# Performance work log

Hardware: AMD Instinct MI355X
Metric: run time of the kernel (lower is better)

Reference implementation:

```python
import jax, jax.numpy as jnp
import numpy as np

DIM = 1024
PRUNE_RATE = 1.0


def setup_inputs() -> dict:
    key = jax.random.key(0)
    k1, k2 = jax.random.split(key)
    x = jax.random.normal(k1, (8, 4096, DIM), dtype=jnp.float32)
    mask_param = jax.random.normal(k2, (DIM,), dtype=jnp.float32)
    _mask = jnp.ones((DIM,), dtype=jnp.float32)
    return {"x": x, "mask_param": mask_param, "_mask": _mask}


def reference(x, mask_param, _mask):
    # get_mask(): prune_rate * dim * softmax(mask) * _mask  (non-fixed branch)
    mask = PRUNE_RATE * DIM * jax.nn.softmax(mask_param, axis=0) * _mask
    # torch.matmul(x, torch.diag(mask)) == per-channel broadcast multiply
    xm = x * mask  # [B, S, D] * [D]
    return (xm, mask)
```

## Files before the change

### kernel.cpp

```cpp
#include <hip/hip_runtime.h>
#include <math.h>

#define DIM 1024

__global__ __launch_bounds__(1024) void mask_softmax_kernel(
    const float* __restrict__ mask_param,
    const float* __restrict__ mask_in,
    float* __restrict__ mask_out)
{
    __shared__ float red[16];
    __shared__ float s_max, s_sum;
    const int t = threadIdx.x;

    const float p = mask_param[t];

    float m = p;
    #pragma unroll
    for (int o = 32; o > 0; o >>= 1) m = fmaxf(m, __shfl_down(m, o, 64));
    if ((t & 63) == 0) red[t >> 6] = m;
    __syncthreads();
    if (t < 16) {
        float mm = red[t];
        #pragma unroll
        for (int o = 8; o > 0; o >>= 1) mm = fmaxf(mm, __shfl_down(mm, o, 16));
        if (t == 0) s_max = mm;
    }
    __syncthreads();

    const float e = expf(p - s_max);
    float s = e;
    #pragma unroll
    for (int o = 32; o > 0; o >>= 1) s += __shfl_down(s, o, 64);
    if ((t & 63) == 0) red[t >> 6] = s;
    __syncthreads();
    if (t < 16) {
        float ss = red[t];
        #pragma unroll
        for (int o = 8; o > 0; o >>= 1) ss += __shfl_down(ss, o, 16);
        if (t == 0) s_sum = ss;
    }
    __syncthreads();

    mask_out[t] = (float)DIM * (e / s_sum) * mask_in[t];
}

__global__ __launch_bounds__(256) void mask_mul_kernel(
    const float4* __restrict__ x,
    const float4* __restrict__ mask4,
    float4* __restrict__ out,
    int n4)
{
    const int idx    = blockIdx.x * 256 + threadIdx.x;
    const int stride = gridDim.x * 256;

    const float4 mv = mask4[idx & 255];

    for (int i = idx; i < n4; i += stride) {
        float4 v = x[i];
        v.x *= mv.x; v.y *= mv.y; v.z *= mv.z; v.w *= mv.w;
        out[i] = v;
    }
}

extern "C" void kernel_launch(void* const* d_in, const int* in_sizes, int n_in,
                              void* d_out, int out_size, void* d_ws, size_t ws_size,
                              hipStream_t stream)
{
    const float* x          = (const float*)d_in[0];
    const float* mask_param = (const float*)d_in[1];
    const float* mask_in    = (const float*)d_in[2];

    const int n = in_sizes[0];
    float* out_xm   = (float*)d_out;
    float* out_mask = (float*)d_out + n;

    mask_softmax_kernel<<<1, 1024, 0, stream>>>(mask_param, mask_in, out_mask);

    const int n4 = n / 4;
    const int blocks = 4096;
    mask_mul_kernel<<<blocks, 256, 0, stream>>>(
        (const float4*)x, (const float4*)out_mask, (float4*)out_xm, n4);
}
```

Measured before the change: 238.5 us.

## Fuse softmax mask computation into the broadcast multiply kernel

Drops the separate single-block softmax kernel. Each block of the multiply kernel now recomputes the 1024-element softmax itself from float4 loads, and block 0 writes the mask output. This removes one kernel launch and the serial dependency between the two kernels. In exchange every block does redundant reductions with two barriers, and the grid doubles to 8192 blocks so each thread handles fewer iterations. __expf also replaces expf, which is less precise.

New measurement: 232.4 us. 1.03x faster.

```diff
diff --git a/kernel.cpp b/kernel.cpp
--- a/kernel.cpp
+++ b/kernel.cpp
@@ -3,58 +3,51 @@
 
 #define DIM 1024
 
-__global__ __launch_bounds__(1024) void mask_softmax_kernel(
-    const float* __restrict__ mask_param,
-    const float* __restrict__ mask_in,
-    float* __restrict__ mask_out)
+__global__ __launch_bounds__(256) void fused_mask_mul_kernel(
+    const float4* __restrict__ x,
+    const float4* __restrict__ mask_param4,
+    const float4* __restrict__ mask_in4,
+    float4* __restrict__ out,
+    float4* __restrict__ mask_out4,
+    int n4)
 {
-    __shared__ float red[16];
-    __shared__ float s_max, s_sum;
     const int t = threadIdx.x;
 
-    const float p = mask_param[t];
+    const float4 p = mask_param4[t];
 
-    float m = p;
+    float m = fmaxf(fmaxf(p.x, p.y), fmaxf(p.z, p.w));
     #pragma unroll
     for (int o = 32; o > 0; o >>= 1) m = fmaxf(m, __shfl_down(m, o, 64));
+    __shared__ float red[4];
+    __shared__ float s_max, s_sum;
     if ((t & 63) == 0) red[t >> 6] = m;
     __syncthreads();
-    if (t < 16) {
-        float mm = red[t];
-        #pragma unroll
-        for (int o = 8; o > 0; o >>= 1) mm = fmaxf(mm, __shfl_down(mm, o, 16));
-        if (t == 0) s_max = mm;
-    }
+    if (t == 0) s_max = fmaxf(fmaxf(red[0], red[1]), fmaxf(red[2], red[3]));
     __syncthreads();
 
-    const float e = expf(p - s_max);
-    float s = e;
+    const float mx = s_max;
+    float4 e;
+    e.x = __expf(p.x - mx); e.y = __expf(p.y - mx);
+    e.z = __expf(p.z - mx); e.w = __expf(p.w - mx);
+
+    float s = e.x + e.y + e.z + e.w;
     #pragma unroll
     for (int o = 32; o > 0; o >>= 1) s += __shfl_down(s, o, 64);
     if ((t & 63) == 0) red[t >> 6] = s;
     __syncthreads();
-    if (t < 16) {
-        float ss = red[t];
-        #pragma unroll
-        for (int o = 8; o > 0; o >>= 1) ss += __shfl_down(ss, o, 16);
-        if (t == 0) s_sum = ss;
-    }
+    if (t == 0) s_sum = red[0] + red[1] + red[2] + red[3];
     __syncthreads();
 
-    mask_out[t] = (float)DIM * (e / s_sum) * mask_in[t];
-}
+    const float scale = (float)DIM / s_sum;
+    const float4 mi = mask_in4[t];
+    float4 mv;
+    mv.x = e.x * scale * mi.x; mv.y = e.y * scale * mi.y;
+    mv.z = e.z * scale * mi.z; mv.w = e.w * scale * mi.w;
 
-__global__ __launch_bounds__(256) void mask_mul_kernel(
-    const float4* __restrict__ x,
-    const float4* __restrict__ mask4,
-    float4* __restrict__ out,
-    int n4)
-{
-    const int idx    = blockIdx.x * 256 + threadIdx.x;
+    if (blockIdx.x == 0) mask_out4[t] = mv;
+
+    const int idx    = blockIdx.x * 256 + t;
     const int stride = gridDim.x * 256;
-
-    const float4 mv = mask4[idx & 255];
-
     for (int i = idx; i < n4; i += stride) {
         float4 v = x[i];
         v.x *= mv.x; v.y *= mv.y; v.z *= mv.z; v.w *= mv.w;
@@ -74,10 +67,9 @@
     float* out_xm   = (float*)d_out;
     float* out_mask = (float*)d_out + n;
 
-    mask_softmax_kernel<<<1, 1024, 0, stream>>>(mask_param, mask_in, out_mask);
-
     const int n4 = n / 4;
-    const int blocks = 4096;
-    mask_mul_kernel<<<blocks, 256, 0, stream>>>(
-        (const float4*)x, (const float4*)out_mask, (float4*)out_xm, n4);
+    const int blocks = 8192;
+    fused_mask_mul_kernel<<<blocks, 256, 0, stream>>>(
+        (const float4*)x, (const float4*)mask_param, (const float4*)mask_in,
+        (float4*)out_xm, (float4*)out_mask, n4);
 }
```
